# Kernel tuning notes

Hardware: AMD Instinct MI355X
Metric: run time of the kernel (lower is better)

Reference implementation:

```python
import jax, jax.numpy as jnp
import numpy as np

EMBED = 1024
HEADS = 16
HEAD_DIM = EMBED // HEADS


def setup_inputs() -> dict:
    key = jax.random.key(0)
    ks = jax.random.split(key, 9)
    s = 1.0 / np.sqrt(EMBED)
    inp = {
        "inputs": jax.random.normal(ks[0], (2, 2048, EMBED), dtype=jnp.float32),
        "Wq": jax.random.normal(ks[1], (EMBED, EMBED), dtype=jnp.float32) * s,
        "bq": jnp.zeros((EMBED,), dtype=jnp.float32),
        "Wk": jax.random.normal(ks[2], (EMBED, EMBED), dtype=jnp.float32) * s,
        "bk": jnp.zeros((EMBED,), dtype=jnp.float32),
        "Wv": jax.random.normal(ks[3], (EMBED, EMBED), dtype=jnp.float32) * s,
        "bv": jnp.zeros((EMBED,), dtype=jnp.float32),
        "Wo": jax.random.normal(ks[4], (EMBED, EMBED), dtype=jnp.float32) * s,
        "bo": jnp.zeros((EMBED,), dtype=jnp.float32),
    }
    return inp


def _split_heads(x, B, S):
    # [B, S, E] -> [B, H, S, D]
    return x.reshape(B, S, HEADS, HEAD_DIM).transpose(0, 2, 1, 3)


def reference(inputs, Wq, bq, Wk, bk, Wv, bv, Wo, bo):
    B, S, E = inputs.shape
    q = _split_heads(inputs @ Wq + bq, B, S)
    k = _split_heads(inputs @ Wk + bk, B, S)
    v = _split_heads(inputs @ Wv + bv, B, S)
    # scaled dot-product attention per the original: score scaled by sqrt(d_k)
    score = jnp.einsum("bhsd,bhtd->bhst", q, k) / jnp.sqrt(jnp.float32(HEAD_DIM))
    weights = jax.nn.softmax(score, axis=-1)
    attn = jnp.einsum("bhst,bhtd->bhsd", weights, v)
    concat = attn.transpose(0, 2, 1, 3).reshape(B, S, E)
    return concat @ Wo + bo
```

## Files before the change

kernel.cpp:

```cpp
#include <hip/hip_runtime.h>
#include <cmath>

#define EMBED 1024
#define HEADS 16
#define HDIM  64
#define BATCH 2
#define SEQ   2048
#define MTOT  (BATCH*SEQ)
#define KDIM  1024

typedef __attribute__((ext_vector_type(8))) short bf16x8;
typedef __attribute__((ext_vector_type(4))) float fx4;

#define MFMA(a,b,c) __builtin_amdgcn_mfma_f32_16x16x32_bf16((a),(b),(c),0,0,0)

__device__ __forceinline__ unsigned short f2bf(float x) {
    unsigned u = __float_as_uint(x);
    unsigned r = (u + 0x7FFFu + ((u >> 16) & 1u)) >> 16;
    return (unsigned short)r;
}
__device__ __forceinline__ float bf2f(unsigned short h) {
    return __uint_as_float(((unsigned)h) << 16);
}
__device__ __forceinline__ int swz_grp(int row, int grp) {
    return row * 64 + ((grp ^ (row & 7)) << 3);
}
__device__ __forceinline__ void gload16(const void* g, void* l) {
    __builtin_amdgcn_global_load_lds((const __attribute__((address_space(1))) void*)g,
                                     (__attribute__((address_space(3))) void*)l, 16, 0, 0);
}
__device__ __forceinline__ float dpp_qswap(float x) {
    return __int_as_float(__builtin_amdgcn_mov_dpp(__float_as_int(x), 0xB1, 0xF, 0xF, true));
}

#define C2S 0.18033688f

__global__ __launch_bounds__(256)
void prep(const float* __restrict__ X,
          const float* __restrict__ Wq, const float* __restrict__ Wk,
          const float* __restrict__ Wv, const float* __restrict__ Wo,
          unsigned short* __restrict__ Xh,
          unsigned short* __restrict__ WtH, unsigned short* __restrict__ WtOh)
{
    const int bid = blockIdx.x;
    const int tid = threadIdx.x;
    if (bid < 2048) {
        int i = (bid * 256 + tid) * 8;
        float4 a = *(const float4*)(X + i);
        float4 b = *(const float4*)(X + i + 4);
        bf16x8 h;
        h[0] = (short)f2bf(a.x); h[1] = (short)f2bf(a.y);
        h[2] = (short)f2bf(a.z); h[3] = (short)f2bf(a.w);
        h[4] = (short)f2bf(b.x); h[5] = (short)f2bf(b.y);
        h[6] = (short)f2bf(b.z); h[7] = (short)f2bf(b.w);
        *(bf16x8*)(Xh + i) = h;
        return;
    }
    const int u = bid - 2048;
    const int z = u >> 8;
    const float* W = (z == 0) ? Wq : (z == 1) ? Wk : (z == 2) ? Wv : Wo;
    unsigned short* Th = (z < 3) ? WtH + (size_t)z * 1048576 : WtOh;
    const int k0 = ((u >> 4) & 15) * 64, n0 = (u & 15) * 64;

    __shared__ float t[64][65];
    #pragma unroll
    for (int it = 0; it < 4; ++it) {
        int v2 = tid + it * 256;
        int r = v2 >> 4, c4 = (v2 & 15) << 2;
        float4 v = *(const float4*)(W + (size_t)(k0 + r) * EMBED + n0 + c4);
        t[r][c4] = v.x; t[r][c4 + 1] = v.y; t[r][c4 + 2] = v.z; t[r][c4 + 3] = v.w;
    }
    __syncthreads();
    #pragma unroll
    for (int it = 0; it < 4; ++it) {
        int v2 = tid + it * 256;
        int r = v2 >> 4, c4 = (v2 & 15) << 2;
        ushort4 h;
        h.x = f2bf(t[c4 + 0][r]);
        h.y = f2bf(t[c4 + 1][r]);
        h.z = f2bf(t[c4 + 2][r]);
        h.w = f2bf(t[c4 + 3][r]);
        *(ushort4*)(Th + (size_t)(n0 + r) * EMBED + k0 + c4) = h;
    }
}

__global__ __launch_bounds__(256, 3)
void gemm_qkv(const unsigned short* __restrict__ Xh,
              const unsigned short* __restrict__ WtH,
              const float* __restrict__ bq, const float* __restrict__ bk,
              const float* __restrict__ bv,
              unsigned short* __restrict__ Qh, unsigned short* __restrict__ Khi,
              unsigned short* __restrict__ Vhi)
{
    __shared__ unsigned short Ah[8192];
    __shared__ unsigned short Bh[8192];

    const int tid = threadIdx.x, lane = tid & 63, w = tid >> 6;
    const int wm = w >> 1, wn = w & 1;
    const int which = blockIdx.y;
    const int lin = (blockIdx.x & 7) * 32 + (blockIdx.x >> 3);
    const int m0 = (lin >> 3) * 128, n0 = (lin & 7) * 128;

    const char* aB = (const char*)(Xh + (size_t)m0 * KDIM);
    const char* bB = (const char*)(WtH + (size_t)which * 1048576 + (size_t)n0 * KDIM);

    auto stageA = [&](int kt) {
        #pragma unroll
        for (int i = 0; i < 4; ++i) {
            int uw = (i << 12) + (w << 10);
            int u  = uw + (lane << 4);
            int row = u >> 7, grp = (u >> 4) & 7;
            size_t gb = (size_t)row * (KDIM * 2) + (size_t)kt * 128 + ((grp ^ (row & 7)) << 4);
            gload16(aB + gb, (char*)Ah + uw);
        }
    };
    auto stageB = [&](int kt) {
        #pragma unroll
        for (int i = 0; i < 4; ++i) {
            int uw = (i << 12) + (w << 10);
            int u  = uw + (lane << 4);
            int row = u >> 7, grp = (u >> 4) & 7;
            size_t gb = (size_t)row * (KDIM * 2) + (size_t)kt * 128 + ((grp ^ (row & 7)) << 4);
            gload16(bB + gb, (char*)Bh + uw);
        }
    };

    const fx4 zero4 = {0.f, 0.f, 0.f, 0.f};
    fx4 acc[4][4];
    #pragma unroll
    for (int i = 0; i < 4; ++i)
        #pragma unroll
        for (int j = 0; j < 4; ++j) acc[i][j] = zero4;

    for (int kt = 0; kt < KDIM / 64; ++kt) {
        __syncthreads();
        stageA(kt);
        stageB(kt);
        __syncthreads();
        #pragma unroll
        for (int kh = 0; kh < 2; ++kh) {
            const int grp = kh * 4 + (lane >> 4);
            bf16x8 ah[4], bh4[4];
            #pragma unroll
            for (int mi = 0; mi < 4; ++mi)
                ah[mi] = *(const bf16x8*)(Ah + swz_grp(wm * 64 + mi * 16 + (lane & 15), grp));
            #pragma unroll
            for (int ni = 0; ni < 4; ++ni)
                bh4[ni] = *(const bf16x8*)(Bh + swz_grp(wn * 64 + ni * 16 + (lane & 15), grp));
            #pragma unroll
            for (int mi = 0; mi < 4; ++mi)
                #pragma unroll
                for (int ni = 0; ni < 4; ++ni)
                    acc[mi][ni] = MFMA(ah[mi], bh4[ni], acc[mi][ni]);
        }
    }

    const float* bias = (which == 0) ? bq : (which == 1) ? bk : bv;
    #pragma unroll
    for (int mi = 0; mi < 4; ++mi)
        #pragma unroll
        for (int ni = 0; ni < 4; ++ni) {
            const int n = n0 + wn * 64 + ni * 16 + (lane & 15);
            const float bb = bias[n];
            const int hh = n >> 6, d = n & 63;
            if (which < 2) {
                unsigned short* plane = (which == 0) ? Qh : Khi;
                #pragma unroll
                for (int reg = 0; reg < 4; ++reg) {
                    const int m = m0 + wm * 64 + mi * 16 + (lane >> 4) * 4 + reg;
                    const int b = m >> 11, s = m & (SEQ - 1);
                    float val = acc[mi][ni][reg] + bb;
                    if (which == 0) val *= C2S;
                    plane[((size_t)(b * HEADS + hh) * SEQ + s) * HDIM + d] = f2bf(val);
                }
            } else {
                const int m = m0 + wm * 64 + mi * 16 + (lane >> 4) * 4;
                const int b = m >> 11, s = m & (SEQ - 1);
                const int sl = s & 63;
                const int c = (sl & 32) | ((sl & 12) << 1) | ((sl & 16) >> 2);
                ushort4 o;
                o.x = f2bf(acc[mi][ni][0] + bb);
                o.y = f2bf(acc[mi][ni][1] + bb);
                o.z = f2bf(acc[mi][ni][2] + bb);
                o.w = f2bf(acc[mi][ni][3] + bb);
                *(ushort4*)(Vhi + ((size_t)(b * HEADS + hh) * HDIM + d) * SEQ
                            + (s & ~63) + c) = o;
            }
        }
}

__global__ __launch_bounds__(256, 4)
void gemm_ao(const unsigned short* __restrict__ AOh,
             const unsigned short* __restrict__ Bgh,
             const float* __restrict__ bias, float* __restrict__ Cf)
{
    __shared__ unsigned short Ah[8192];
    __shared__ unsigned short Bh[4096];

    const int tid = threadIdx.x, lane = tid & 63, w = tid >> 6;
    const int wm = w >> 1, wn = w & 1;
    const int lin = (blockIdx.x & 7) * 64 + (blockIdx.x >> 3);
    const int m0 = (lin >> 4) * 128, n0 = (lin & 15) * 64;

    const char* aB = (const char*)(AOh + (size_t)m0 * KDIM);
    const char* bB = (const char*)(Bgh + (size_t)n0 * KDIM);

    auto stageA = [&](int kt) {
        #pragma unroll
        for (int i = 0; i < 4; ++i) {
            int uw = (i << 12) + (w << 10);
            int u  = uw + (lane << 4);
            int row = u >> 7, grp = (u >> 4) & 7;
            size_t gb = (size_t)row * (KDIM * 2) + (size_t)kt * 128 + ((grp ^ (row & 7)) << 4);
            gload16(aB + gb, (char*)Ah + uw);
        }
    };
    auto stageB = [&](int kt) {
        #pragma unroll
        for (int i = 0; i < 2; ++i) {
            int uw = (i << 12) + (w << 10);
            int u  = uw + (lane << 4);
            int row = u >> 7, grp = (u >> 4) & 7;
            size_t gb = (size_t)row * (KDIM * 2) + (size_t)kt * 128 + ((grp ^ (row & 7)) << 4);
            gload16(bB + gb, (char*)Bh + uw);
        }
    };

    const fx4 zero4 = {0.f, 0.f, 0.f, 0.f};
    fx4 acc[4][2];
    #pragma unroll
    for (int i = 0; i < 4; ++i) { acc[i][0] = zero4; acc[i][1] = zero4; }

    for (int kt = 0; kt < KDIM / 64; ++kt) {
        __syncthreads();
        stageA(kt);
        stageB(kt);
        __syncthreads();
        #pragma unroll
        for (int kh = 0; kh < 2; ++kh) {
            const int grp = kh * 4 + (lane >> 4);
            bf16x8 ah[4], bh2[2];
            #pragma unroll
            for (int mi = 0; mi < 4; ++mi)
                ah[mi] = *(const bf16x8*)(Ah + swz_grp(wm * 64 + mi * 16 + (lane & 15), grp));
            #pragma unroll
            for (int ni = 0; ni < 2; ++ni)
                bh2[ni] = *(const bf16x8*)(Bh + swz_grp(wn * 32 + ni * 16 + (lane & 15), grp));
            #pragma unroll
            for (int mi = 0; mi < 4; ++mi)
                #pragma unroll
                for (int ni = 0; ni < 2; ++ni)
                    acc[mi][ni] = MFMA(ah[mi], bh2[ni], acc[mi][ni]);
        }
    }

    #pragma unroll
    for (int mi = 0; mi < 4; ++mi)
        #pragma unroll
        for (int ni = 0; ni < 2; ++ni) {
            const int n = n0 + wn * 32 + ni * 16 + (lane & 15);
            const float bb = bias[n];
            #pragma unroll
            for (int reg = 0; reg < 4; ++reg) {
                const int m = m0 + wm * 64 + mi * 16 + (lane >> 4) * 4 + reg;
                Cf[(size_t)m * EMBED + n] = acc[mi][ni][reg] + bb;
            }
        }
}

__global__ __launch_bounds__(512, 8)
void attn_mfma(const unsigned short* __restrict__ Qh,
               const unsigned short* __restrict__ Khi,
               const unsigned short* __restrict__ Vhi, unsigned short* __restrict__ AOh)
{
    __shared__ unsigned short Ks[2][4096];
    __shared__ unsigned short Vs[2][4096];

    const int tid = threadIdx.x, lane = tid & 63, w = tid >> 6;
    const int xcd = blockIdx.x & 7, loc = blockIdx.x >> 3;
    const int bh = xcd * 4 + (loc >> 4);
    const int q0 = (loc & 15) * 128;
    const size_t qkBase = (size_t)bh * SEQ * HDIM;

    auto stageKV = [&](int kv0, int buf) {
        const char* baseK = (const char*)(Khi + qkBase + (size_t)kv0 * HDIM);
        const char* baseV = (const char*)(Vhi + (size_t)bh * HDIM * SEQ + kv0);
        const int uw = w << 10;
        const int u  = uw + (lane << 4);
        const int row = u >> 7, grp = (u >> 4) & 7;
        const size_t gk = (size_t)row * 128 + ((grp ^ (row & 7)) << 4);
        const size_t gv = (size_t)row * (SEQ * 2) + ((grp ^ (row & 7)) << 4);
        gload16(baseK + gk, (char*)Ks[buf] + uw);
        gload16(baseV + gv, (char*)Vs[buf] + uw);
    };

    bf16x8 qf[2];
    #pragma unroll
    for (int kh = 0; kh < 2; ++kh) {
        const int row = q0 + w * 16 + (lane & 15);
        const int grp = kh * 4 + (lane >> 4);
        qf[kh] = *(const bf16x8*)(Qh + qkBase + (size_t)row * HDIM + grp * 8);
    }

    const fx4 zero4 = {0.f, 0.f, 0.f, 0.f};
    fx4 acco[4];
    fx4 accl = zero4;
    #pragma unroll
    for (int df = 0; df < 4; ++df) acco[df] = zero4;

    bf16x8 ones;
    #pragma unroll
    for (int i = 0; i < 8; ++i) ones[i] = (short)0x3F80;

    stageKV(0, 0);
    __syncthreads();

    for (int t = 0; t < 32; ++t) {
        const int cur = t & 1;
        if (t < 31) stageKV((t + 1) * 64, cur ^ 1);

        fx4 s4[4] = {zero4, zero4, zero4, zero4};
        __builtin_amdgcn_s_setprio(1);
        #pragma unroll
        for (int kh = 0; kh < 2; ++kh) {
            const int grp = kh * 4 + (lane >> 4);
            bf16x8 kf[4];
            #pragma unroll
            for (int nf = 0; nf < 4; ++nf)
                kf[nf] = *(const bf16x8*)(Ks[cur] + swz_grp(nf * 16 + (lane & 15), grp));
            #pragma unroll
            for (int nf = 0; nf < 4; ++nf)
                s4[nf] = MFMA(kf[nf], qf[kh], s4[nf]);
        }
        __builtin_amdgcn_s_setprio(0);

        float p[4][4];
        #pragma unroll
        for (int kvf = 0; kvf < 4; ++kvf)
            #pragma unroll
            for (int reg = 0; reg < 4; ++reg) {
                float e;
                asm("v_exp_f32 %0, %1\n\ts_nop 0" : "=v"(e) : "v"(s4[kvf][reg]));
                p[kvf][reg] = e;
            }

        bf16x8 pa[2];
        #pragma unroll
        for (int t2 = 0; t2 < 2; ++t2) {
            union { unsigned u[4]; bf16x8 v; } pk;
            asm("v_cvt_pk_bf16_f32 %0, %1, %2" : "=v"(pk.u[0])
                : "v"(p[2 * t2][0]), "v"(p[2 * t2][1]));
            asm("v_cvt_pk_bf16_f32 %0, %1, %2" : "=v"(pk.u[1])
                : "v"(p[2 * t2][2]), "v"(p[2 * t2][3]));
            asm("v_cvt_pk_bf16_f32 %0, %1, %2" : "=v"(pk.u[2])
                : "v"(p[2 * t2 + 1][0]), "v"(p[2 * t2 + 1][1]));
            asm("v_cvt_pk_bf16_f32 %0, %1, %2" : "=v"(pk.u[3])
                : "v"(p[2 * t2 + 1][2]), "v"(p[2 * t2 + 1][3]));
            pa[t2] = pk.v;
        }

        __builtin_amdgcn_s_setprio(1);
        #pragma unroll
        for (int t2 = 0; t2 < 2; ++t2) {
            const int grp = t2 * 4 + (lane >> 4);
            accl = MFMA(pa[t2], ones, accl);
            #pragma unroll
            for (int df = 0; df < 4; ++df) {
                bf16x8 vh = *(const bf16x8*)(Vs[cur] + swz_grp(df * 16 + (lane & 15), grp));
                acco[df] = MFMA(pa[t2], vh, acco[df]);
            }
        }
        __builtin_amdgcn_s_setprio(0);

        __syncthreads();
    }

    const int b = bh >> 4, h = bh & 15;
    const int parity = lane & 1;
    float inv[4];
    #pragma unroll
    for (int reg = 0; reg < 4; ++reg) inv[reg] = __builtin_amdgcn_rcpf(accl[reg]);
    #pragma unroll
    for (int df = 0; df < 4; ++df) {
        const int d0 = df * 16 + ((lane & 15) & ~1);
        #pragma unroll
        for (int rp = 0; rp < 4; rp += 2) {
            float ve = acco[df][rp]     * inv[rp];
            float vo = acco[df][rp + 1] * inv[rp + 1];
            float e_sw = dpp_qswap(ve), o_sw = dpp_qswap(vo);
            float a  = parity ? o_sw : ve;
            float b2 = parity ? vo   : e_sw;
            unsigned u;
            asm volatile("v_cvt_pk_bf16_f32 %0, %1, %2" : "=v"(u) : "v"(a), "v"(b2));
            const int q = q0 + w * 16 + (lane >> 4) * 4 + rp + parity;
            *(unsigned int*)(AOh + ((size_t)(b * SEQ + q) * EMBED + h * HDIM + d0)) = u;
        }
    }
}

extern "C" void kernel_launch(void* const* d_in, const int* in_sizes, int n_in,
                              void* d_out, int out_size, void* d_ws, size_t ws_size,
                              hipStream_t stream)
{
    (void)in_sizes; (void)n_in; (void)out_size; (void)ws_size;

    const float* X  = (const float*)d_in[0];
    const float* Wq = (const float*)d_in[1];
    const float* bq = (const float*)d_in[2];
    const float* Wk = (const float*)d_in[3];
    const float* bk = (const float*)d_in[4];
    const float* Wv = (const float*)d_in[5];
    const float* bv = (const float*)d_in[6];
    const float* Wo = (const float*)d_in[7];
    const float* bo = (const float*)d_in[8];

    const size_t R_us = (size_t)8 * 1024 * 1024;
    unsigned short* us = (unsigned short*)d_ws;
    unsigned short* Qh   = us + 0 * R_us;
    unsigned short* WtOh = us + 0 * R_us + 4194304;
    unsigned short* Khi  = us + 1 * R_us;
    unsigned short* Vhi  = us + 2 * R_us;
    unsigned short* AOh  = us + 3 * R_us;
    unsigned short* WtH  = us + 3 * R_us;
    unsigned short* Xh   = (unsigned short*)d_out;

    prep<<<dim3(3072), dim3(256), 0, stream>>>(X, Wq, Wk, Wv, Wo, Xh, WtH, WtOh);

    gemm_qkv<<<dim3(256, 3), dim3(256), 0, stream>>>(Xh, WtH, bq, bk, bv, Qh, Khi, Vhi);

    attn_mfma<<<dim3(512), dim3(512), 0, stream>>>(Qh, Khi, Vhi, AOh);

    gemm_ao<<<dim3(512), dim3(256), 0, stream>>>(AOh, WtOh, bo, (float*)d_out);
}
```

Before: 101.8 us.

## Enlarge per-warp tiles in attention and output GEMM to increase fragment reuse

```diff
diff --git a/kernel.cpp b/kernel.cpp
--- a/kernel.cpp
+++ b/kernel.cpp
@@ -189,18 +189,18 @@
         }
 }
 
-__global__ __launch_bounds__(256, 4)
+__global__ __launch_bounds__(256, 3)
 void gemm_ao(const unsigned short* __restrict__ AOh,
              const unsigned short* __restrict__ Bgh,
              const float* __restrict__ bias, float* __restrict__ Cf)
 {
     __shared__ unsigned short Ah[8192];
-    __shared__ unsigned short Bh[4096];
+    __shared__ unsigned short Bh[8192];
 
     const int tid = threadIdx.x, lane = tid & 63, w = tid >> 6;
     const int wm = w >> 1, wn = w & 1;
-    const int lin = (blockIdx.x & 7) * 64 + (blockIdx.x >> 3);
-    const int m0 = (lin >> 4) * 128, n0 = (lin & 15) * 64;
+    const int lin = (blockIdx.x & 7) * 32 + (blockIdx.x >> 3);
+    const int m0 = (lin >> 3) * 128, n0 = (lin & 7) * 128;
 
     const char* aB = (const char*)(AOh + (size_t)m0 * KDIM);
     const char* bB = (const char*)(Bgh + (size_t)n0 * KDIM);
@@ -217,7 +217,7 @@
     };
     auto stageB = [&](int kt) {
         #pragma unroll
-        for (int i = 0; i < 2; ++i) {
+        for (int i = 0; i < 4; ++i) {
             int uw = (i << 12) + (w << 10);
             int u  = uw + (lane << 4);
             int row = u >> 7, grp = (u >> 4) & 7;
@@ -227,9 +227,11 @@
     };
 
     const fx4 zero4 = {0.f, 0.f, 0.f, 0.f};
-    fx4 acc[4][2];
-    #pragma unroll
-    for (int i = 0; i < 4; ++i) { acc[i][0] = zero4; acc[i][1] = zero4; }
+    fx4 acc[4][4];
+    #pragma unroll
+    for (int i = 0; i < 4; ++i)
+        #pragma unroll
+        for (int j = 0; j < 4; ++j) acc[i][j] = zero4;
 
     for (int kt = 0; kt < KDIM / 64; ++kt) {
         __syncthreads();
@@ -239,26 +241,26 @@
         #pragma unroll
         for (int kh = 0; kh < 2; ++kh) {
             const int grp = kh * 4 + (lane >> 4);
-            bf16x8 ah[4], bh2[2];
+            bf16x8 ah[4], bh4[4];
             #pragma unroll
             for (int mi = 0; mi < 4; ++mi)
                 ah[mi] = *(const bf16x8*)(Ah + swz_grp(wm * 64 + mi * 16 + (lane & 15), grp));
             #pragma unroll
-            for (int ni = 0; ni < 2; ++ni)
-                bh2[ni] = *(const bf16x8*)(Bh + swz_grp(wn * 32 + ni * 16 + (lane & 15), grp));
+            for (int ni = 0; ni < 4; ++ni)
+                bh4[ni] = *(const bf16x8*)(Bh + swz_grp(wn * 64 + ni * 16 + (lane & 15), grp));
             #pragma unroll
             for (int mi = 0; mi < 4; ++mi)
                 #pragma unroll
-                for (int ni = 0; ni < 2; ++ni)
-                    acc[mi][ni] = MFMA(ah[mi], bh2[ni], acc[mi][ni]);
+                for (int ni = 0; ni < 4; ++ni)
+                    acc[mi][ni] = MFMA(ah[mi], bh4[ni], acc[mi][ni]);
         }
     }
 
     #pragma unroll
     for (int mi = 0; mi < 4; ++mi)
         #pragma unroll
-        for (int ni = 0; ni < 2; ++ni) {
-            const int n = n0 + wn * 32 + ni * 16 + (lane & 15);
+        for (int ni = 0; ni < 4; ++ni) {
+            const int n = n0 + wn * 64 + ni * 16 + (lane & 15);
             const float bb = bias[n];
             #pragma unroll
             for (int reg = 0; reg < 4; ++reg) {
@@ -268,7 +270,7 @@
         }
 }
 
-__global__ __launch_bounds__(512, 8)
+__global__ __launch_bounds__(256, 2)
 void attn_mfma(const unsigned short* __restrict__ Qh,
                const unsigned short* __restrict__ Khi,
                const unsigned short* __restrict__ Vhi, unsigned short* __restrict__ AOh)
@@ -285,28 +287,35 @@
     auto stageKV = [&](int kv0, int buf) {
         const char* baseK = (const char*)(Khi + qkBase + (size_t)kv0 * HDIM);
         const char* baseV = (const char*)(Vhi + (size_t)bh * HDIM * SEQ + kv0);
-        const int uw = w << 10;
-        const int u  = uw + (lane << 4);
-        const int row = u >> 7, grp = (u >> 4) & 7;
-        const size_t gk = (size_t)row * 128 + ((grp ^ (row & 7)) << 4);
-        const size_t gv = (size_t)row * (SEQ * 2) + ((grp ^ (row & 7)) << 4);
-        gload16(baseK + gk, (char*)Ks[buf] + uw);
-        gload16(baseV + gv, (char*)Vs[buf] + uw);
+        #pragma unroll
+        for (int i = 0; i < 2; ++i) {
+            int uw = (i << 12) + (w << 10);
+            int u  = uw + (lane << 4);
+            int row = u >> 7, grp = (u >> 4) & 7;
+            size_t gk = (size_t)row * 128 + ((grp ^ (row & 7)) << 4);
+            size_t gv = (size_t)row * (SEQ * 2) + ((grp ^ (row & 7)) << 4);
+            gload16(baseK + gk, (char*)Ks[buf] + uw);
+            gload16(baseV + gv, (char*)Vs[buf] + uw);
+        }
     };
 
-    bf16x8 qf[2];
-    #pragma unroll
-    for (int kh = 0; kh < 2; ++kh) {
-        const int row = q0 + w * 16 + (lane & 15);
-        const int grp = kh * 4 + (lane >> 4);
-        qf[kh] = *(const bf16x8*)(Qh + qkBase + (size_t)row * HDIM + grp * 8);
-    }
+    bf16x8 qf[2][2];
+    #pragma unroll
+    for (int kh = 0; kh < 2; ++kh)
+        #pragma unroll
+        for (int mi = 0; mi < 2; ++mi) {
+            const int row = q0 + w * 32 + mi * 16 + (lane & 15);
+            const int grp = kh * 4 + (lane >> 4);
+            qf[kh][mi] = *(const bf16x8*)(Qh + qkBase + (size_t)row * HDIM + grp * 8);
+        }
 
     const fx4 zero4 = {0.f, 0.f, 0.f, 0.f};
-    fx4 acco[4];
-    fx4 accl = zero4;
-    #pragma unroll
-    for (int df = 0; df < 4; ++df) acco[df] = zero4;
+    fx4 acco[2][4];
+    fx4 accl[2] = {zero4, zero4};
+    #pragma unroll
+    for (int mi = 0; mi < 2; ++mi)
+        #pragma unroll
+        for (int df = 0; df < 4; ++df) acco[mi][df] = zero4;
 
     bf16x8 ones;
     #pragma unroll
@@ -319,7 +328,11 @@
         const int cur = t & 1;
         if (t < 31) stageKV((t + 1) * 64, cur ^ 1);
 
-        fx4 s4[4] = {zero4, zero4, zero4, zero4};
+        fx4 s4[2][4];
+        #pragma unroll
+        for (int mi = 0; mi < 2; ++mi)
+            #pragma unroll
+            for (int nf = 0; nf < 4; ++nf) s4[mi][nf] = zero4;
         __builtin_amdgcn_s_setprio(1);
         #pragma unroll
         for (int kh = 0; kh < 2; ++kh) {
@@ -329,45 +342,53 @@
             for (int nf = 0; nf < 4; ++nf)
                 kf[nf] = *(const bf16x8*)(Ks[cur] + swz_grp(nf * 16 + (lane & 15), grp));
             #pragma unroll
-            for (int nf = 0; nf < 4; ++nf)
-                s4[nf] = MFMA(kf[nf], qf[kh], s4[nf]);
+            for (int mi = 0; mi < 2; ++mi)
+                #pragma unroll
+                for (int nf = 0; nf < 4; ++nf)
+                    s4[mi][nf] = MFMA(kf[nf], qf[kh][mi], s4[mi][nf]);
         }
         __builtin_amdgcn_s_setprio(0);
 
-        float p[4][4];
-        #pragma unroll
-        for (int kvf = 0; kvf < 4; ++kvf)
-            #pragma unroll
-            for (int reg = 0; reg < 4; ++reg) {
-                float e;
-                asm("v_exp_f32 %0, %1\n\ts_nop 0" : "=v"(e) : "v"(s4[kvf][reg]));
-                p[kvf][reg] = e;
+        bf16x8 pa[2][2];
+        #pragma unroll
+        for (int mi = 0; mi < 2; ++mi) {
+            float p[4][4];
+            #pragma unroll
+            for (int kvf = 0; kvf < 4; ++kvf)
+                #pragma unroll
+                for (int reg = 0; reg < 4; ++reg) {
+                    float e;
+                    asm("v_exp_f32 %0, %1\n\ts_nop 0" : "=v"(e) : "v"(s4[mi][kvf][reg]));
+                    p[kvf][reg] = e;
+                }
+            #pragma unroll
+            for (int t2 = 0; t2 < 2; ++t2) {
+                union { unsigned u[4]; bf16x8 v; } pk;
+                asm("v_cvt_pk_bf16_f32 %0, %1, %2" : "=v"(pk.u[0])
+                    : "v"(p[2 * t2][0]), "v"(p[2 * t2][1]));
+                asm("v_cvt_pk_bf16_f32 %0, %1, %2" : "=v"(pk.u[1])
+                    : "v"(p[2 * t2][2]), "v"(p[2 * t2][3]));
+                asm("v_cvt_pk_bf16_f32 %0, %1, %2" : "=v"(pk.u[2])
+                    : "v"(p[2 * t2 + 1][0]), "v"(p[2 * t2 + 1][1]));
+                asm("v_cvt_pk_bf16_f32 %0, %1, %2" : "=v"(pk.u[3])
+                    : "v"(p[2 * t2 + 1][2]), "v"(p[2 * t2 + 1][3]));
+                pa[mi][t2] = pk.v;
             }
-
-        bf16x8 pa[2];
-        #pragma unroll
-        for (int t2 = 0; t2 < 2; ++t2) {
-            union { unsigned u[4]; bf16x8 v; } pk;
-            asm("v_cvt_pk_bf16_f32 %0, %1, %2" : "=v"(pk.u[0])
-                : "v"(p[2 * t2][0]), "v"(p[2 * t2][1]));
-            asm("v_cvt_pk_bf16_f32 %0, %1, %2" : "=v"(pk.u[1])
-                : "v"(p[2 * t2][2]), "v"(p[2 * t2][3]));
-            asm("v_cvt_pk_bf16_f32 %0, %1, %2" : "=v"(pk.u[2])
-                : "v"(p[2 * t2 + 1][0]), "v"(p[2 * t2 + 1][1]));
-            asm("v_cvt_pk_bf16_f32 %0, %1, %2" : "=v"(pk.u[3])
-                : "v"(p[2 * t2 + 1][2]), "v"(p[2 * t2 + 1][3]));
-            pa[t2] = pk.v;
         }
 
         __builtin_amdgcn_s_setprio(1);
         #pragma unroll
         for (int t2 = 0; t2 < 2; ++t2) {
             const int grp = t2 * 4 + (lane >> 4);
-            accl = MFMA(pa[t2], ones, accl);
+            #pragma unroll
+            for (int mi = 0; mi < 2; ++mi)
+                accl[mi] = MFMA(pa[mi][t2], ones, accl[mi]);
             #pragma unroll
             for (int df = 0; df < 4; ++df) {
                 bf16x8 vh = *(const bf16x8*)(Vs[cur] + swz_grp(df * 16 + (lane & 15), grp));
-                acco[df] = MFMA(pa[t2], vh, acco[df]);
+                #pragma unroll
+                for (int mi = 0; mi < 2; ++mi)
+                    acco[mi][df] = MFMA(pa[mi][t2], vh, acco[mi][df]);
             }
         }
         __builtin_amdgcn_s_setprio(0);
@@ -377,23 +398,26 @@
 
     const int b = bh >> 4, h = bh & 15;
     const int parity = lane & 1;
-    float inv[4];
-    #pragma unroll
-    for (int reg = 0; reg < 4; ++reg) inv[reg] = __builtin_amdgcn_rcpf(accl[reg]);
-    #pragma unroll
-    for (int df = 0; df < 4; ++df) {
-        const int d0 = df * 16 + ((lane & 15) & ~1);
-        #pragma unroll
-        for (int rp = 0; rp < 4; rp += 2) {
-            float ve = acco[df][rp]     * inv[rp];
-            float vo = acco[df][rp + 1] * inv[rp + 1];
-            float e_sw = dpp_qswap(ve), o_sw = dpp_qswap(vo);
-            float a  = parity ? o_sw : ve;
-            float b2 = parity ? vo   : e_sw;
-            unsigned u;
-            asm volatile("v_cvt_pk_bf16_f32 %0, %1, %2" : "=v"(u) : "v"(a), "v"(b2));
-            const int q = q0 + w * 16 + (lane >> 4) * 4 + rp + parity;
-            *(unsigned int*)(AOh + ((size_t)(b * SEQ + q) * EMBED + h * HDIM + d0)) = u;
+    #pragma unroll
+    for (int mi = 0; mi < 2; ++mi) {
+        float inv[4];
+        #pragma unroll
+        for (int reg = 0; reg < 4; ++reg) inv[reg] = __builtin_amdgcn_rcpf(accl[mi][reg]);
+        #pragma unroll
+        for (int df = 0; df < 4; ++df) {
+            const int d0 = df * 16 + ((lane & 15) & ~1);
+            #pragma unroll
+            for (int rp = 0; rp < 4; rp += 2) {
+                float ve = acco[mi][df][rp]     * inv[rp];
+                float vo = acco[mi][df][rp + 1] * inv[rp + 1];
+                float e_sw = dpp_qswap(ve), o_sw = dpp_qswap(vo);
+                float a  = parity ? o_sw : ve;
+                float b2 = parity ? vo   : e_sw;
+                unsigned u;
+                asm volatile("v_cvt_pk_bf16_f32 %0, %1, %2" : "=v"(u) : "v"(a), "v"(b2));
+                const int q = q0 + w * 32 + mi * 16 + (lane >> 4) * 4 + rp + parity;
+                *(unsigned int*)(AOh + ((size_t)(b * SEQ + q) * EMBED + h * HDIM + d0)) = u;
+            }
         }
     }
 }
@@ -428,7 +452,7 @@
 
     gemm_qkv<<<dim3(256, 3), dim3(256), 0, stream>>>(Xh, WtH, bq, bk, bv, Qh, Khi, Vhi);
 
-    attn_mfma<<<dim3(512), dim3(512), 0, stream>>>(Qh, Khi, Vhi, AOh);
-
-    gemm_ao<<<dim3(512), dim3(256), 0, stream>>>(AOh, WtOh, bo, (float*)d_out);
-}
+    attn_mfma<<<dim3(512), dim3(256), 0, stream>>>(Qh, Khi, Vhi, AOh);
+
+    gemm_ao<<<dim3(256), dim3(256), 0, stream>>>(AOh, WtOh, bo, (float*)d_out);
+}
```

Measured after the change: 104.7 us. 2.9% more time.
